# Kernel tuning notes

Measured on AMD Instinct MI355X. Metric: run time of the kernel, lower is better.

The kernel has to match this reference:

```python
import jax, jax.numpy as jnp
import numpy as np

DIM = 1024      # feature_size
K = 128         # num_clusters
E = 2           # expansion
G = 8           # groups
ITERN = 3       # Newton-Schulz iterations
DG = E * DIM // G  # 256 per-group dim


def setup_inputs() -> dict:
    key = jax.random.key(0)
    ks = jax.random.split(key, 10)
    f32 = jnp.float32
    return {
        "x": jax.random.normal(ks[0], (32, DIM, 16, 8), dtype=f32),
        "centroids": jax.random.normal(ks[1], (K, DG), dtype=f32) * 0.05,
        "W_inp": jax.random.normal(ks[2], (E * DIM, DIM), dtype=f32) * 0.02,
        "b_inp": jax.random.normal(ks[3], (E * DIM,), dtype=f32) * 0.01,
        "W_g": jax.random.normal(ks[4], (G, E * DIM), dtype=f32) * 0.02,
        "b_g": jax.random.normal(ks[5], (G,), dtype=f32) * 0.01,
        "W_gk": jax.random.normal(ks[6], (G * K, E * DIM), dtype=f32) * 0.02,
        "b_gk": jax.random.normal(ks[7], (G * K,), dtype=f32) * 0.01,
        "W_f": jax.random.normal(ks[8], (1, K), dtype=f32) * 0.05,
        "b_f": jax.random.normal(ks[9], (1,), dtype=f32) * 0.01,
    }


def _covpool(v):
    # v: [bs, d, h, w] -> second-order pooling [bs, d, d]; x @ I_hat @ x^T == centered outer product / M
    bs, d = v.shape[0], v.shape[1]
    m = v.shape[2] * v.shape[3]
    v = v.reshape(bs, d, m)
    vc = v - v.mean(axis=2, keepdims=True)
    return jnp.einsum('bdm,bem->bde', vc, vc) / m


def _sqrtm_ns(cov, iter_n):
    # MPNCOV Newton-Schulz matrix square root (iter_n >= 2)
    d = cov.shape[1]
    I3 = 3.0 * jnp.eye(d, dtype=cov.dtype)[None]
    norm_a = jnp.trace(cov, axis1=1, axis2=2)[:, None, None]  # pre-normalization by trace
    A = cov / norm_a
    ZY = 0.5 * (I3 - A)
    Y = A @ ZY
    Z = ZY
    for _ in range(1, iter_n - 1):
        ZY = 0.5 * (I3 - Z @ Y)
        Y, Z = Y @ ZY, ZY @ Z
    ZY = 0.5 * (Y @ (I3 - Z @ Y))
    return ZY * jnp.sqrt(norm_a)


def _triuvec(cov):
    # row-major upper-triangular (incl. diagonal) vectorization, matching MPNCOV Triuvec
    d = cov.shape[1]
    r, c = np.triu_indices(d)
    return cov[:, r, c]


def reference(x, centroids, W_inp, b_inp, W_g, b_g, W_gk, b_gk, W_f, b_f):
    resolution = x.shape[-1]
    b8, C, H, W = x.shape
    bs = b8 // 8
    # [bs*8, C, H, W] -> [bs, M, N] with M = 8*H*W, N = C
    xt = x.reshape(bs, 8, C, H, W).transpose(0, 2, 1, 3, 4).reshape(bs, C, 8 * H * W)
    xt = jnp.transpose(xt, (0, 2, 1))
    M = xt.shape[1]
    # L2-normalize along feature dim (F.normalize eps clamp)
    xt = xt / jnp.maximum(jnp.linalg.norm(xt, axis=2, keepdims=True), 1e-12)
    h = xt @ W_inp.T + b_inp                               # [bs, M, E*N]
    alpha_g = jax.nn.sigmoid(h @ W_g.T + b_g)              # [bs, M, G]
    alpha_gk = jax.nn.softmax(h @ W_gk.T + b_gk, axis=1)   # NOTE: nn.Softmax(dim=1) -> over M
    alpha_gk = alpha_gk.reshape(bs, M, G, K)
    rx = h.reshape(bs, M, G, DG)                           # [bs, M, G, DG]
    w = alpha_g[..., None] * alpha_gk                      # [bs, M, G, K]
    # fused residual-weighted sum over M: sum_m w*(x - c) = (sum_m w*x) - (sum_m w)*c
    vlad = jnp.einsum('bmgk,bmgd->bgkd', w, rx) - w.sum(axis=1)[..., None] * centroids
    # learnable fusion over clusters K
    vf = jnp.einsum('bgkd,k->bgd', vlad, W_f[0]) + b_f[0]  # [bs, G, DG]
    vf = jnp.transpose(vf, (0, 2, 1))                      # [bs, DG, G]
    vf = vf.reshape(bs, DG, G // resolution, resolution)
    cov = _covpool(vf)
    cov = _sqrtm_ns(cov, ITERN)
    return _triuvec(cov)                                   # [bs, DG*(DG+1)//2]
```

## Files before the change

### kernel.cpp

```cpp
#include <hip/hip_runtime.h>
#include <math.h>

typedef float f32x4 __attribute__((ext_vector_type(4)));
typedef short bf16x8 __attribute__((ext_vector_type(8)));
typedef unsigned short u16;

__device__ __forceinline__ u16 f2bf(float f) {
    unsigned u = __builtin_bit_cast(unsigned, f);
    u += 0x7fff + ((u >> 16) & 1);
    return (u16)(u >> 16);
}
__device__ __forceinline__ float bf2f(u16 s) {
    unsigned v = ((unsigned)s) << 16;
    return __builtin_bit_cast(float, v);
}
__device__ __forceinline__ void gload16(const void* g, void* l) {
    __builtin_amdgcn_global_load_lds(
        (const __attribute__((address_space(1))) unsigned int*)g,
        (__attribute__((address_space(3))) unsigned int*)l, 16, 0, 0);
}

__global__ __launch_bounds__(256) void k_f2bf2(const float* __restrict__ a,
                                               const float* __restrict__ b,
                                               u16* __restrict__ out, int na, int n) {
    int i = (blockIdx.x * 256 + threadIdx.x) * 4;
    if (i < n) {
        const float* src = (i < na) ? (a + i) : (b + (i - na));
        float4 v = *(const float4*)src;
        ushort4 o;
        o.x = f2bf(v.x); o.y = f2bf(v.y); o.z = f2bf(v.z); o.w = f2bf(v.w);
        *(ushort4*)(out + i) = o;
    }
}

__global__ __launch_bounds__(256) void k_transpose_norm(const float* __restrict__ x,
                                                        u16* __restrict__ xtn) {
    int b8 = blockIdx.x;
    int hh = blockIdx.y;
    int tid = threadIdx.x;
    __shared__ float tile[8][1032];
    __shared__ float inv[8];
    const float* src = x + (size_t)b8 * 1024 * 128 + hh * 8;
    #pragma unroll
    for (int r = 0; r < 4; ++r) {
        int c = tid * 4 + r;
        const float* p = src + (size_t)c * 128;
        float4 v0 = *(const float4*)(p);
        float4 v1 = *(const float4*)(p + 4);
        tile[0][c] = v0.x; tile[1][c] = v0.y; tile[2][c] = v0.z; tile[3][c] = v0.w;
        tile[4][c] = v1.x; tile[5][c] = v1.y; tile[6][c] = v1.z; tile[7][c] = v1.w;
    }
    __syncthreads();
    int w = tid >> 5, j = tid & 31;
    float s = 0.f;
    #pragma unroll 8
    for (int i = 0; i < 32; ++i) { float v = tile[w][i * 32 + j]; s += v * v; }
    #pragma unroll
    for (int m = 16; m; m >>= 1) s += __shfl_xor(s, m);
    if (j == 0) inv[w] = 1.0f / fmaxf(sqrtf(s), 1e-12f);
    __syncthreads();
    int b = b8 >> 3, t = b8 & 7;
    int c0 = tid * 4;
    for (int w2 = 0; w2 < 8; ++w2) {
        int m = t * 128 + hh * 8 + w2;
        float sc = inv[w2];
        u16* dst = xtn + ((size_t)b * 1024 + m) * 1024;
        ushort4 o;
        o.x = f2bf(tile[w2][c0 + 0] * sc);
        o.y = f2bf(tile[w2][c0 + 1] * sc);
        o.z = f2bf(tile[w2][c0 + 2] * sc);
        o.w = f2bf(tile[w2][c0 + 3] * sc);
        *(ushort4*)(dst + c0) = o;
    }
}

template <int MODE>
__global__ __launch_bounds__(256) void k_mfma_gemm(
    const u16* __restrict__ A, const u16* __restrict__ B,
    float* __restrict__ Cf, u16* __restrict__ Cb,
    const float* __restrict__ bias, int K, int N,
    long long Bstr, long long Cstr)
{
    int bz = blockIdx.z;
    B += (size_t)bz * Bstr;
    int tid = threadIdx.x, lane = tid & 63, wave = tid >> 6;
    int wr = wave >> 1, wc = wave & 1;
    int i0 = blockIdx.y * 128, j0 = blockIdx.x * 128;
    __shared__ u16 As[3][128 * 32];
    __shared__ u16 Bs[3][128 * 32];
    f32x4 acc[4][4] = {};
    int lrow = lane >> 2;
    int lk = ((lane & 3) ^ ((lane >> 3) & 3)) * 8;
    int fr = lane & 15, fg = lane >> 4;
    int ca = (fg ^ ((fr >> 1) & 3)) * 8;

    auto stage = [&](int buf, int t) {
        int kt = t << 5;
        #pragma unroll
        for (int q = 0; q < 2; ++q) {
            int blk = q * 4 + wave;
            gload16(A + (size_t)(i0 + blk * 16 + lrow) * K + kt + lk, &As[buf][blk * 512]);
            gload16(B + (size_t)(j0 + blk * 16 + lrow) * K + kt + lk, &Bs[buf][blk * 512]);
        }
    };
    auto compute = [&](int buf) {
        bf16x8 af[4], bv[4];
        #pragma unroll
        for (int mi = 0; mi < 4; ++mi)
            af[mi] = *(const bf16x8*)&As[buf][(wr * 64 + mi * 16 + fr) * 32 + ca];
        #pragma unroll
        for (int ni = 0; ni < 4; ++ni)
            bv[ni] = *(const bf16x8*)&Bs[buf][(wc * 64 + ni * 16 + fr) * 32 + ca];
        #pragma unroll
        for (int mi = 0; mi < 4; ++mi)
            #pragma unroll
            for (int ni = 0; ni < 4; ++ni)
                acc[mi][ni] = __builtin_amdgcn_mfma_f32_16x16x32_bf16(
                    af[mi], bv[ni], acc[mi][ni], 0, 0, 0);
    };

    int nk = K >> 5;
    stage(0, 0);
    stage(1, 1);
    int cur = 0;
    for (int t = 0; t < nk; ++t) {
        if (t + 2 < nk) {
            int nb = cur + 2; if (nb >= 3) nb -= 3;
            stage(nb, t + 2);
            asm volatile("s_waitcnt vmcnt(8)" ::: "memory");
        } else if (t + 1 < nk) {
            asm volatile("s_waitcnt vmcnt(4)" ::: "memory");
        } else {
            asm volatile("s_waitcnt vmcnt(0)" ::: "memory");
        }
        __builtin_amdgcn_s_barrier();
        compute(cur);
        __builtin_amdgcn_s_barrier();
        ++cur; if (cur == 3) cur = 0;
    }

    if (MODE == 1) {
        #pragma unroll
        for (int ni = 0; ni < 4; ++ni) {
            int col = j0 + wc * 64 + ni * 16 + fr;
            float bvv = bias[col];
            #pragma unroll
            for (int mi = 0; mi < 4; ++mi)
                #pragma unroll
                for (int r = 0; r < 4; ++r) {
                    int row = i0 + wr * 64 + mi * 16 + fg * 4 + r;
                    Cb[(size_t)row * N + col] = f2bf(acc[mi][ni][r] + bvv);
                }
        }
    } else {
        float* C2 = Cf + (size_t)bz * Cstr;
        #pragma unroll
        for (int ni = 0; ni < 4; ++ni) {
            int col = j0 + wc * 64 + ni * 16 + fr;
            #pragma unroll
            for (int mi = 0; mi < 4; ++mi)
                #pragma unroll
                for (int r = 0; r < 4; ++r) {
                    int row = i0 + wr * 64 + mi * 16 + fg * 4 + r;
                    C2[(size_t)row * N + col] = acc[mi][ni][r];
                }
        }
    }
}

__global__ __launch_bounds__(256) void k_alpha_g(const u16* __restrict__ h,
                                                 const float* __restrict__ Wg,
                                                 const float* __restrict__ bg,
                                                 float* __restrict__ agT) {
    __shared__ float wgl[16384];
    int tid = threadIdx.x;
    #pragma unroll
    for (int i = 0; i < 16; ++i) {
        int idx = tid * 4 + i * 1024;
        *(float4*)&wgl[idx] = *(const float4*)&Wg[idx];
    }
    __syncthreads();
    float bgl[8];
    #pragma unroll
    for (int g = 0; g < 8; ++g) bgl[g] = bg[g];
    int wv = tid >> 6, lane = tid & 63;
    int bm0 = blockIdx.x * 16;
    for (int r = 0; r < 4; ++r) {
        int bm = bm0 + wv * 4 + r;
        const u16* hr = h + (size_t)bm * 2048;
        float acc[8] = {};
        #pragma unroll
        for (int i = 0; i < 4; ++i) {
            int c0 = i * 512 + lane * 8;
            bf16x8 hv8 = *(const bf16x8*)(hr + c0);
            float hf[8];
            #pragma unroll
            for (int j = 0; j < 8; ++j) hf[j] = bf2f((u16)hv8[j]);
            #pragma unroll
            for (int g = 0; g < 8; ++g) {
                const float* wrp = &wgl[g * 2048 + c0];
                #pragma unroll
                for (int j = 0; j < 8; ++j) acc[g] += hf[j] * wrp[j];
            }
        }
        #pragma unroll
        for (int g = 0; g < 8; ++g) {
            #pragma unroll
            for (int off = 32; off; off >>= 1) acc[g] += __shfl_xor(acc[g], off);
        }
        if (lane < 8) {
            int b = bm >> 10, m = bm & 1023;
            agT[((size_t)b * 8 + lane) * 1024 + m] =
                1.f / (1.f + expf(-(acc[lane] + bgl[lane])));
        }
    }
}

__global__ __launch_bounds__(256) void k_softmax(float* __restrict__ lt,
                                                 const float* __restrict__ agT,
                                                 float* __restrict__ wsum) {
    int gk = blockIdx.x, b = blockIdx.y;
    int tid = threadIdx.x;
    float* row = lt + ((size_t)b * 1024 + gk) * 1024;
    int g = gk >> 7;
    const float* ag = agT + ((size_t)b * 8 + g) * 1024;
    __shared__ float red[4], red2[4], red3[4];
    float4 v = *(const float4*)(row + tid * 4);
    float mx = fmaxf(fmaxf(v.x, v.y), fmaxf(v.z, v.w));
    #pragma unroll
    for (int m = 32; m; m >>= 1) mx = fmaxf(mx, __shfl_xor(mx, m));
    if ((tid & 63) == 0) red[tid >> 6] = mx;
    __syncthreads();
    mx = fmaxf(fmaxf(red[0], red[1]), fmaxf(red[2], red[3]));
    float e0 = expf(v.x - mx), e1 = expf(v.y - mx), e2 = expf(v.z - mx), e3 = expf(v.w - mx);
    float s = e0 + e1 + e2 + e3;
    #pragma unroll
    for (int m = 32; m; m >>= 1) s += __shfl_xor(s, m);
    if ((tid & 63) == 0) red2[tid >> 6] = s;
    __syncthreads();
    s = red2[0] + red2[1] + red2[2] + red2[3];
    float invs = 1.f / s;
    float4 a = *(const float4*)(ag + tid * 4);
    float w0 = e0 * invs * a.x, w1 = e1 * invs * a.y, w2 = e2 * invs * a.z, w3 = e3 * invs * a.w;
    float4 o; o.x = w0; o.y = w1; o.z = w2; o.w = w3;
    *(float4*)(row + tid * 4) = o;
    float t = w0 + w1 + w2 + w3;
    #pragma unroll
    for (int m = 32; m; m >>= 1) t += __shfl_xor(t, m);
    if ((tid & 63) == 0) red3[tid >> 6] = t;
    __syncthreads();
    if (tid == 0) wsum[((size_t)b * 8 + g) * 128 + (gk & 127)] = red3[0] + red3[1] + red3[2] + red3[3];
}

__global__ __launch_bounds__(256) void k_wf_u(const float* __restrict__ wT,
                                              const float* __restrict__ wsum,
                                              const float* __restrict__ Wf,
                                              float* __restrict__ wf, float* __restrict__ u) {
    int ms = blockIdx.x, bg = blockIdx.y;
    int tid = threadIdx.x;
    __shared__ float wfl[128];
    __shared__ float part[256];
    if (tid < 128) {
        wfl[tid] = Wf[tid];
        if (ms == 0) u[bg * 128 + tid] = Wf[tid] * wsum[bg * 128 + tid];
    }
    __syncthreads();
    int ml = tid & 127;
    int kh = tid >> 7;
    const float* base = wT + (size_t)bg * 131072 + (size_t)kh * 64 * 1024 + ms * 128;
    float acc = 0.f;
    #pragma unroll 4
    for (int k = 0; k < 64; ++k) acc += wfl[kh * 64 + k] * base[(size_t)k * 1024 + ml];
    part[tid] = acc;
    __syncthreads();
    if (tid < 128) wf[(size_t)bg * 1024 + ms * 128 + ml] = part[tid] + part[tid + 128];
}

__global__ __launch_bounds__(256) void k_vf_partial(const u16* __restrict__ h,
                                                    const float* __restrict__ wf,
                                                    const float* __restrict__ u,
                                                    const float* __restrict__ cent,
                                                    float* __restrict__ vfp) {
    int mc = blockIdx.x;
    int g = blockIdx.y, b = blockIdx.z;
    int d = threadIdx.x;
    __shared__ float wl[64];
    __shared__ float ul[128];
    float acc = 0.f;
    if (mc < 16) {
        if (d < 64) wl[d] = wf[((size_t)b * 8 + g) * 1024 + mc * 64 + d];
        __syncthreads();
        const u16* hb = h + (size_t)b * 1024 * 2048 + (size_t)(mc * 64) * 2048 + g * 256;
        #pragma unroll 4
        for (int m = 0; m < 64; ++m) acc += wl[m] * bf2f(hb[(size_t)m * 2048 + d]);
    } else {
        if (d < 128) ul[d] = u[((size_t)b * 8 + g) * 128 + d];
        __syncthreads();
        for (int k = 0; k < 128; ++k) acc -= ul[k] * cent[k * 256 + d];
    }
    vfp[(((size_t)b * 8 + g) * 17 + mc) * 256 + d] = acc;
}

#define MM8(DST, P, Q) do { if (act) { float s_ = 0.f; \
    _Pragma("unroll") \
    for (int l_ = 0; l_ < 8; ++l_) s_ += P[ii][l_] * Q[l_][jj]; \
    DST[ii][jj] = s_; } __syncthreads(); } while (0)

__global__ __launch_bounds__(256) void k_finalize(const float* __restrict__ vfp,
                                                  const float* __restrict__ bf,
                                                  float* __restrict__ VcOut,
                                                  float* __restrict__ Wrow,
                                                  float* __restrict__ s0) {
    int b = blockIdx.x;
    int tid = threadIdx.x;
    __shared__ float Vl[256][9];
    __shared__ float red[256];
    __shared__ float Sm[8][8], W1[8][8], W2[8][8], YmL[8][8], ZmL[8][8], ZYL[8][8], FmL[8][8];
    int d = tid;
    float bfv = bf[0];
    float vfl[8];
    #pragma unroll
    for (int g = 0; g < 8; ++g) {
        float acc = 0.f;
        for (int mc = 0; mc < 17; ++mc)
            acc += vfp[(((size_t)b * 8 + g) * 17 + mc) * 256 + d];
        vfl[g] = acc + bfv;
    }
    float mean = 0.f;
    #pragma unroll
    for (int g = 0; g < 8; ++g) mean += vfl[g];
    mean *= 0.125f;
    float trp = 0.f;
    #pragma unroll
    for (int g = 0; g < 8; ++g) { float v = vfl[g] - mean; Vl[d][g] = v; trp += v * v; }
    red[tid] = trp;
    __syncthreads();
    for (int s = 128; s > 0; s >>= 1) { if (tid < s) red[tid] += red[tid + s]; __syncthreads(); }
    float tr = red[0] * 0.125f;
    bool act = tid < 64;
    int ii = (tid >> 3) & 7, jj = tid & 7;
    if (act) {
        float sv = 0.f;
        for (int dd = 0; dd < 256; ++dd) sv += Vl[dd][ii] * Vl[dd][jj];
        Sm[ii][jj] = sv / (8.f * tr);
    }
    __syncthreads();
    if (act) {
        YmL[ii][jj] = (ii == jj ? 1.5f : 0.f) - 0.5f * Sm[ii][jj];
        ZmL[ii][jj] = (ii == jj ? -0.5f : 0.f);
    }
    __syncthreads();
    float ya = 0.f, za = 1.5f;
    MM8(W1, Sm, YmL);
    MM8(W2, ZmL, W1);
    float pa = za * ya;
    if (act) ZYL[ii][jj] = -0.5f * (za * YmL[ii][jj] + ya * ZmL[ii][jj] + W2[ii][jj]);
    __syncthreads();
    float zya = 1.5f - 0.5f * pa;
    MM8(W1, Sm, ZYL);
    MM8(W2, YmL, W1);
    if (act) YmL[ii][jj] = ya * ZYL[ii][jj] + zya * YmL[ii][jj] + W2[ii][jj];
    __syncthreads();
    ya = ya * zya;
    MM8(W1, Sm, ZmL);
    MM8(W2, ZYL, W1);
    if (act) ZmL[ii][jj] = zya * ZmL[ii][jj] + za * ZYL[ii][jj] + W2[ii][jj];
    __syncthreads();
    za = zya * za;
    MM8(W1, Sm, YmL);
    MM8(W2, ZmL, W1);
    float p2a = za * ya;
    if (act) ZYL[ii][jj] = za * YmL[ii][jj] + ya * ZmL[ii][jj] + W2[ii][jj];
    __syncthreads();
    MM8(W1, Sm, ZYL);
    MM8(W2, YmL, W1);
    if (act) FmL[ii][jj] = 0.5f * ((3.f - p2a) * YmL[ii][jj] - ya * ZYL[ii][jj] - W2[ii][jj]);
    __syncthreads();
    float fa = 0.5f * ya * (3.f - p2a);
    float sqtr = sqrtf(tr);
    float scaleF = 1.f / (8.f * sqtr);
    #pragma unroll
    for (int jo = 0; jo < 8; ++jo) {
        float sv = 0.f;
        #pragma unroll
        for (int i = 0; i < 8; ++i) sv += Vl[d][i] * FmL[i][jo];
        Wrow[((size_t)b * 256 + d) * 8 + jo] = sv * scaleF;
    }
    #pragma unroll
    for (int jo = 0; jo < 8; ++jo) VcOut[((size_t)b * 256 + d) * 8 + jo] = Vl[d][jo];
    if (tid == 0) s0[b] = fa * sqtr;
}

__global__ __launch_bounds__(256) void k_output(const float* __restrict__ Vc,
                                                const float* __restrict__ Wrow,
                                                const float* __restrict__ s0,
                                                float* __restrict__ out) {
    int dd = blockIdx.x, b = blockIdx.y;
    int e = threadIdx.x;
    __shared__ float Vl[256][9];
    __shared__ float wr[8];
    float4 v0 = *(const float4*)(Vc + ((size_t)b * 256 + e) * 8);
    float4 v1 = *(const float4*)(Vc + ((size_t)b * 256 + e) * 8 + 4);
    Vl[e][0] = v0.x; Vl[e][1] = v0.y; Vl[e][2] = v0.z; Vl[e][3] = v0.w;
    Vl[e][4] = v1.x; Vl[e][5] = v1.y; Vl[e][6] = v1.z; Vl[e][7] = v1.w;
    if (e < 8) wr[e] = Wrow[((size_t)b * 256 + dd) * 8 + e];
    __syncthreads();
    if (e >= dd) {
        float v = (e == dd) ? s0[b] : 0.f;
        #pragma unroll
        for (int j = 0; j < 8; ++j) v += wr[j] * Vl[e][j];
        size_t idx = (size_t)b * 32896 + (size_t)dd * 256 - ((size_t)dd * (dd - 1)) / 2 + (e - dd);
        out[idx] = v;
    }
}

extern "C" void kernel_launch(void* const* d_in, const int* in_sizes, int n_in,
                              void* d_out, int out_size, void* d_ws, size_t ws_size,
                              hipStream_t stream) {
    const float* x    = (const float*)d_in[0];
    const float* cent = (const float*)d_in[1];
    const float* Winp = (const float*)d_in[2];
    const float* binp = (const float*)d_in[3];
    const float* Wg   = (const float*)d_in[4];
    const float* bg   = (const float*)d_in[5];
    const float* Wgk  = (const float*)d_in[6];
    const float* Wf   = (const float*)d_in[8];
    const float* bf   = (const float*)d_in[9];
    float* out = (float*)d_out;
    char* wsb = (char*)d_ws;

    float* lt    = (float*)(wsb);
    u16*   xtnb  = (u16*)(wsb);
    u16*   hb    = (u16*)(wsb + (16ull << 20));
    u16*   winpb = (u16*)(wsb + (32ull << 20));
    u16*   wgkb  = (u16*)(wsb + (36ull << 20));
    float* agT   = (float*)(wsb + (40ull << 20));
    float* wsum  = agT + 32768;
    float* wf    = wsum + 4096;
    float* u     = wf + 32768;
    float* vfp   = u + 4096;
    float* Vc    = vfp + 139264;
    float* Wr    = Vc + 8192;
    float* s0    = Wr + 8192;

    k_transpose_norm<<<dim3(32, 16), 256, 0, stream>>>(x, xtnb);
    k_f2bf2<<<4096, 256, 0, stream>>>(Winp, Wgk, winpb, 2097152, 4194304);
    k_mfma_gemm<1><<<dim3(16, 32, 1), 256, 0, stream>>>(
        xtnb, winpb, nullptr, hb, binp, 1024, 2048, 0, 0);
    k_alpha_g<<<256, 256, 0, stream>>>(hb, Wg, bg, agT);
    k_mfma_gemm<0><<<dim3(8, 8, 4), 256, 0, stream>>>(
        wgkb, hb, lt, nullptr, nullptr, 2048, 1024, 2097152LL, 1048576LL);
    k_softmax<<<dim3(1024, 4), 256, 0, stream>>>(lt, agT, wsum);
    k_wf_u<<<dim3(8, 32), 256, 0, stream>>>(lt, wsum, Wf, wf, u);
    k_vf_partial<<<dim3(17, 8, 4), 256, 0, stream>>>(hb, wf, u, cent, vfp);
    k_finalize<<<4, 256, 0, stream>>>(vfp, bf, Vc, Wr, s0);
    k_output<<<dim3(256, 4), 256, 0, stream>>>(Vc, Wr, s0, out);
}
```

Baseline: 131.5 us.

## Retile MFMA GEMM to 512 threads, BK=64 double buffer, merge batched GEMM

The bf16 MFMA GEMM is rewritten as a templated kernel with 512 threads, K-tile 64, double buffering instead of triple buffering, and a new XOR swizzle for shared memory. The first GEMM uses 256x128 tiles. The second GEMM no longer launches one batch per z-slice; it runs as a single GEMM with N=4096 over all batches, and the layout of the logits buffer changes to [gk][b*1024+m]. Softmax and the wf reduction are updated to index the new layout. The goal is more reuse per tile, fewer barriers, and fewer launches, at the cost of higher LDS and register pressure per block.

```diff
diff --git a/kernel.cpp b/kernel.cpp
--- a/kernel.cpp
+++ b/kernel.cpp
@@ -74,95 +74,110 @@
     }
 }
 
-template <int MODE>
-__global__ __launch_bounds__(256) void k_mfma_gemm(
+template <int BM, int BN, int WC, int MODE>
+__global__ __launch_bounds__(512) void k_mfma_gemm(
     const u16* __restrict__ A, const u16* __restrict__ B,
     float* __restrict__ Cf, u16* __restrict__ Cb,
-    const float* __restrict__ bias, int K, int N,
-    long long Bstr, long long Cstr)
+    const float* __restrict__ bias, int K, int N)
 {
-    int bz = blockIdx.z;
-    B += (size_t)bz * Bstr;
+    constexpr int WR = 8 / WC;
+    constexpr int WM = BM / WR;
+    constexpr int WN = BN / WC;
+    constexpr int MR = WM / 16;
+    constexpr int NR = WN / 16;
+    constexpr int QA = BM / 64;
+    constexpr int QB = BN / 64;
+    constexpr int S = QA + QB;
+    __shared__ u16 As[2][BM * 64];
+    __shared__ u16 Bs[2][BN * 64];
     int tid = threadIdx.x, lane = tid & 63, wave = tid >> 6;
-    int wr = wave >> 1, wc = wave & 1;
-    int i0 = blockIdx.y * 128, j0 = blockIdx.x * 128;
-    __shared__ u16 As[3][128 * 32];
-    __shared__ u16 Bs[3][128 * 32];
-    f32x4 acc[4][4] = {};
-    int lrow = lane >> 2;
-    int lk = ((lane & 3) ^ ((lane >> 3) & 3)) * 8;
+    int wr = wave / WC, wc = wave % WC;
+    int i0 = blockIdx.y * BM, j0 = blockIdx.x * BN;
     int fr = lane & 15, fg = lane >> 4;
-    int ca = (fg ^ ((fr >> 1) & 3)) * 8;
+    f32x4 acc[MR][NR] = {};
+
+    int srcOff = ((tid & 7) ^ ((tid >> 3) & 7)) * 8;
 
     auto stage = [&](int buf, int t) {
-        int kt = t << 5;
-        #pragma unroll
-        for (int q = 0; q < 2; ++q) {
-            int blk = q * 4 + wave;
-            gload16(A + (size_t)(i0 + blk * 16 + lrow) * K + kt + lk, &As[buf][blk * 512]);
-            gload16(B + (size_t)(j0 + blk * 16 + lrow) * K + kt + lk, &Bs[buf][blk * 512]);
+        int kt = t * 64;
+        #pragma unroll
+        for (int q = 0; q < QA; ++q) {
+            int row = (q * 512 + tid) >> 3;
+            gload16(A + (size_t)(i0 + row) * K + kt + srcOff,
+                    &As[buf][(q * 512 + wave * 64) * 8]);
+        }
+        #pragma unroll
+        for (int q = 0; q < QB; ++q) {
+            int row = (q * 512 + tid) >> 3;
+            gload16(B + (size_t)(j0 + row) * K + kt + srcOff,
+                    &Bs[buf][(q * 512 + wave * 64) * 8]);
         }
     };
     auto compute = [&](int buf) {
-        bf16x8 af[4], bv[4];
-        #pragma unroll
-        for (int mi = 0; mi < 4; ++mi)
-            af[mi] = *(const bf16x8*)&As[buf][(wr * 64 + mi * 16 + fr) * 32 + ca];
-        #pragma unroll
-        for (int ni = 0; ni < 4; ++ni)
-            bv[ni] = *(const bf16x8*)&Bs[buf][(wc * 64 + ni * 16 + fr) * 32 + ca];
-        #pragma unroll
-        for (int mi = 0; mi < 4; ++mi)
-            #pragma unroll
-            for (int ni = 0; ni < 4; ++ni)
-                acc[mi][ni] = __builtin_amdgcn_mfma_f32_16x16x32_bf16(
-                    af[mi], bv[ni], acc[mi][ni], 0, 0, 0);
+        #pragma unroll
+        for (int h = 0; h < 2; ++h) {
+            bf16x8 af[MR], bv[NR];
+            #pragma unroll
+            for (int mi = 0; mi < MR; ++mi) {
+                int row = wr * WM + mi * 16 + fr;
+                af[mi] = *(const bf16x8*)&As[buf][row * 64 + ((h * 4 + fg) ^ (fr & 7)) * 8];
+            }
+            #pragma unroll
+            for (int ni = 0; ni < NR; ++ni) {
+                int row = wc * WN + ni * 16 + fr;
+                bv[ni] = *(const bf16x8*)&Bs[buf][row * 64 + ((h * 4 + fg) ^ (fr & 7)) * 8];
+            }
+            #pragma unroll
+            for (int mi = 0; mi < MR; ++mi)
+                #pragma unroll
+                for (int ni = 0; ni < NR; ++ni)
+                    acc[mi][ni] = __builtin_amdgcn_mfma_f32_16x16x32_bf16(
+                        af[mi], bv[ni], acc[mi][ni], 0, 0, 0);
+        }
     };
 
-    int nk = K >> 5;
+    int nk = K >> 6;
     stage(0, 0);
-    stage(1, 1);
     int cur = 0;
     for (int t = 0; t < nk; ++t) {
-        if (t + 2 < nk) {
-            int nb = cur + 2; if (nb >= 3) nb -= 3;
-            stage(nb, t + 2);
-            asm volatile("s_waitcnt vmcnt(8)" ::: "memory");
-        } else if (t + 1 < nk) {
-            asm volatile("s_waitcnt vmcnt(4)" ::: "memory");
+        if (t + 1 < nk) {
+            stage(cur ^ 1, t + 1);
+            if constexpr (S == 6)       asm volatile("s_waitcnt vmcnt(6)" ::: "memory");
+            else if constexpr (S == 4)  asm volatile("s_waitcnt vmcnt(4)" ::: "memory");
+            else                        asm volatile("s_waitcnt vmcnt(8)" ::: "memory");
         } else {
             asm volatile("s_waitcnt vmcnt(0)" ::: "memory");
         }
         __builtin_amdgcn_s_barrier();
+        __builtin_amdgcn_sched_barrier(0);
         compute(cur);
         __builtin_amdgcn_s_barrier();
-        ++cur; if (cur == 3) cur = 0;
+        cur ^= 1;
     }
 
     if (MODE == 1) {
         #pragma unroll
-        for (int ni = 0; ni < 4; ++ni) {
-            int col = j0 + wc * 64 + ni * 16 + fr;
+        for (int ni = 0; ni < NR; ++ni) {
+            int col = j0 + wc * WN + ni * 16 + fr;
             float bvv = bias[col];
             #pragma unroll
-            for (int mi = 0; mi < 4; ++mi)
+            for (int mi = 0; mi < MR; ++mi)
                 #pragma unroll
                 for (int r = 0; r < 4; ++r) {
-                    int row = i0 + wr * 64 + mi * 16 + fg * 4 + r;
+                    int row = i0 + wr * WM + mi * 16 + fg * 4 + r;
                     Cb[(size_t)row * N + col] = f2bf(acc[mi][ni][r] + bvv);
                 }
         }
     } else {
-        float* C2 = Cf + (size_t)bz * Cstr;
-        #pragma unroll
-        for (int ni = 0; ni < 4; ++ni) {
-            int col = j0 + wc * 64 + ni * 16 + fr;
-            #pragma unroll
-            for (int mi = 0; mi < 4; ++mi)
+        #pragma unroll
+        for (int ni = 0; ni < NR; ++ni) {
+            int col = j0 + wc * WN + ni * 16 + fr;
+            #pragma unroll
+            for (int mi = 0; mi < MR; ++mi)
                 #pragma unroll
                 for (int r = 0; r < 4; ++r) {
-                    int row = i0 + wr * 64 + mi * 16 + fg * 4 + r;
-                    C2[(size_t)row * N + col] = acc[mi][ni][r];
+                    int row = i0 + wr * WM + mi * 16 + fg * 4 + r;
+                    Cf[(size_t)row * N + col] = acc[mi][ni][r];
                 }
         }
     }
@@ -221,7 +236,7 @@
                                                  float* __restrict__ wsum) {
     int gk = blockIdx.x, b = blockIdx.y;
     int tid = threadIdx.x;
-    float* row = lt + ((size_t)b * 1024 + gk) * 1024;
+    float* row = lt + (size_t)gk * 4096 + b * 1024;
     int g = gk >> 7;
     const float* ag = agT + ((size_t)b * 8 + g) * 1024;
     __shared__ float red[4], red2[4], red3[4];
@@ -257,6 +272,7 @@
                                               const float* __restrict__ Wf,
                                               float* __restrict__ wf, float* __restrict__ u) {
     int ms = blockIdx.x, bg = blockIdx.y;
+    int b = bg >> 3, g = bg & 7;
     int tid = threadIdx.x;
     __shared__ float wfl[128];
     __shared__ float part[256];
@@ -267,10 +283,10 @@
     __syncthreads();
     int ml = tid & 127;
     int kh = tid >> 7;
-    const float* base = wT + (size_t)bg * 131072 + (size_t)kh * 64 * 1024 + ms * 128;
+    const float* base = wT + (size_t)(g * 128 + kh * 64) * 4096 + (size_t)b * 1024 + ms * 128;
     float acc = 0.f;
     #pragma unroll 4
-    for (int k = 0; k < 64; ++k) acc += wfl[kh * 64 + k] * base[(size_t)k * 1024 + ml];
+    for (int k = 0; k < 64; ++k) acc += wfl[kh * 64 + k] * base[(size_t)k * 4096 + ml];
     part[tid] = acc;
     __syncthreads();
     if (tid < 128) wf[(size_t)bg * 1024 + ms * 128 + ml] = part[tid] + part[tid + 128];
@@ -445,11 +461,11 @@
 
     k_transpose_norm<<<dim3(32, 16), 256, 0, stream>>>(x, xtnb);
     k_f2bf2<<<4096, 256, 0, stream>>>(Winp, Wgk, winpb, 2097152, 4194304);
-    k_mfma_gemm<1><<<dim3(16, 32, 1), 256, 0, stream>>>(
-        xtnb, winpb, nullptr, hb, binp, 1024, 2048, 0, 0);
+    k_mfma_gemm<256, 128, 2, 1><<<dim3(16, 16), 512, 0, stream>>>(
+        xtnb, winpb, nullptr, hb, binp, 1024, 2048);
     k_alpha_g<<<256, 256, 0, stream>>>(hb, Wg, bg, agT);
-    k_mfma_gemm<0><<<dim3(8, 8, 4), 256, 0, stream>>>(
-        wgkb, hb, lt, nullptr, nullptr, 2048, 1024, 2097152LL, 1048576LL);
+    k_mfma_gemm<128, 128, 4, 0><<<dim3(32, 8), 512, 0, stream>>>(
+        wgkb, hb, lt, nullptr, nullptr, 2048, 4096);
     k_softmax<<<dim3(1024, 4), 256, 0, stream>>>(lt, agT, wsum);
     k_wf_u<<<dim3(8, 32), 256, 0, stream>>>(lt, wsum, Wf, wf, u);
     k_vf_partial<<<dim3(17, 8, 4), 256, 0, stream>>>(hb, wf, u, cent, vfp);
```

Result: faster. 123.9 us (-5.8%).
